# Kernel tuning notes

Hardware: AMD Instinct MI355X
Metric: run time of the kernel (lower is better)

The kernel has to match this reference:

```python
import jax, jax.numpy as jnp
import numpy as np

INPUT_SHIFT = 0.1
K = 3  # extract_image_patches(x, 3) hardcodes 3x3 patches


def extract_image_patches(x, k):
    # x: [B, C, H, W] -> [B, k*k*C, Ho, Wo], patch ordering (kh, kw, C)
    B, C, H, W = x.shape
    Ho, Wo = H - k + 1, W - k + 1
    slices = [x[:, :, i:i + Ho, j:j + Wo] for i in range(k) for j in range(k)]
    return jnp.concatenate(slices, axis=1)


def smooth_max(z, axis):
    # SMorph smooth maximum: sum(z * softmax(z)) along axis
    w = jax.nn.softmax(z, axis=axis)
    return jnp.sum(z * w, axis=axis)


def _branch(logp, kflat):
    # logp: [B, P, Ho, Wo]; kflat: [P, O] -> [B, O, Ho, Wo]
    z = logp[:, :, None] + kflat[None, :, :, None, None]  # [B, P, O, Ho, Wo]
    return jnp.exp(smooth_max(z, axis=1))


def setup_inputs() -> dict:
    key = jax.random.key(0)
    kx, kk1, kk2 = jax.random.split(key, 3)
    B, C, H, W, O = 4, 32, 32, 32, 64
    fan_in = K * K * C
    fan_out = K * K * O
    limit = float(np.sqrt(6.0 / (fan_in + fan_out)))  # xavier_uniform
    x = jax.random.normal(kx, (B, C, H, W), dtype=jnp.float32)
    k1 = jax.random.uniform(kk1, (K, K, C, O), minval=-limit, maxval=limit, dtype=jnp.float32)
    k2 = jax.random.uniform(kk2, (K, K, C, O), minval=-limit, maxval=limit, dtype=jnp.float32)
    bias = jnp.zeros((O,), dtype=jnp.float32)
    return {"x": x, "k1": k1, "k2": k2, "bias": bias}


def reference(x, k1, k2, bias):
    kh, kw, C, O = k1.shape
    k1f = k1.reshape(kh * kw * C, O)
    k2f = k2.reshape(kh * kw * C, O)
    # log of clamped patches for +x and -x
    p1 = jnp.log(jnp.maximum(extract_image_patches(x, K), INPUT_SHIFT))
    p2 = jnp.log(jnp.maximum(extract_image_patches(-x, K), INPUT_SHIFT))
    y11 = _branch(p1, k1f)
    y12 = _branch(p1, k2f)
    y21 = _branch(p2, k1f)
    y22 = _branch(p2, k2f)
    return y11 - y12 - y21 + y22 + bias[None, :, None, None]
```

## Files before the change

### kernel.cpp

```cpp
#include <hip/hip_runtime.h>
#include <math.h>


typedef float  f32x4 __attribute__((ext_vector_type(4)));
typedef short  s16x8 __attribute__((ext_vector_type(8)));

#define BB   4
#define CC   32
#define HH   32
#define WW   32
#define OO   64
#define HO   30
#define WO   30
#define NSP  900
#define KDIM 576

#define T1   131072
#define T2   (T1 + 518400)
#define T3   (T2 + 18432)

__device__ __forceinline__ unsigned short f2bf(float f) {
    unsigned u = __float_as_uint(f);
    return (unsigned short)((u + 0x7FFFu + ((u >> 16) & 1u)) >> 16);
}

__global__ __launch_bounds__(256) void smorph_prep(
    const float* __restrict__ x, const float* __restrict__ k1,
    const float* __restrict__ k2, float4* __restrict__ pixs,
    uint4* __restrict__ A3, unsigned short* __restrict__ bt)
{
    const int t = blockIdx.x * 256 + threadIdx.x;

    if (t < T1) {
        const int pix = t >> 5, c = t & 31;
        const int b = pix >> 10, h = (pix >> 5) & 31, w = pix & 31;
        float v = x[b*32768 + c*1024 + h*32 + w];
        float mp = fmaxf(v, 0.1f), mn = fmaxf(-v, 0.1f);
        float lp = mp * logf(mp), ln_ = mn * logf(mn);
        float s0 = mp, s1 = lp, s2 = mn, s3 = ln_;
#pragma unroll
        for (int m = 16; m >= 1; m >>= 1) {
            s0 += __shfl_xor(s0, m); s1 += __shfl_xor(s1, m);
            s2 += __shfl_xor(s2, m); s3 += __shfl_xor(s3, m);
        }
        if (c == 0) pixs[pix] = make_float4(s0, s1, s2, s3);
    } else if (t < T2) {
        const int u   = t - T1;
        const int mt  = u / 2304, rem = u - mt*2304;
        const int st  = rem >> 7, rem2 = rem & 127;
        const int mi  = rem2 >> 6, l = rem2 & 63;
        const int lr  = l & 15, lg = l >> 4;
        const int s   = mt*16 + mi*8 + (lr >> 1);
        const int sign = lr & 1;
        const int pos = st >> 1, khalf = st & 1;
        const int kh  = pos / 3, kw = pos - 3*(pos/3);
        const int b   = s / NSP, r = s - b*NSP;
        const int ho  = r / WO,  wo = r - WO*(r/WO);
        const int h   = ho + kh, w = wo + kw;
        const int c0  = khalf*16 + lg*4;
        const int base = b*32768 + h*32 + w;
        unsigned pk[4];
#pragma unroll
        for (int q = 0; q < 4; ++q) {
            float v = x[base + (c0 + q)*1024];
            float m = sign ? fmaxf(-v, 0.1f) : fmaxf(v, 0.1f);
            pk[q] = (unsigned)f2bf(m) | ((unsigned)f2bf(m * __logf(m)) << 16);
        }
        A3[u] = make_uint4(pk[0], pk[1], pk[2], pk[3]);
    } else if (t < T3) {
        const int u3 = t - T2;
        const int o = u3 & 63, p = u3 >> 6;
        const float a = k1[u3], b2 = k2[u3];
        const float d1 = expm1f(a),  q1 = a  * expf(a);
        const float d2 = expm1f(b2), q2 = b2 * expf(b2);
        const float vals[4][2] = {{d1, 0.f}, {q1, d1}, {d2, 0.f}, {q2, d2}};
#pragma unroll
        for (int tbl = 0; tbl < 4; ++tbl) {
            const int n = o*4 + tbl;
#pragma unroll
            for (int ks = 0; ks < 2; ++ks) {
                const int k    = 2*p + ks;
                const int st   = k >> 5, k32 = k & 31;
                const int lane = (n & 15) + ((k32 >> 3) << 4);
                bt[((n >> 4)*18 + st)*512 + lane*8 + (k32 & 7)] = f2bf(vals[tbl][ks]);
            }
        }
    }
}

__global__ __launch_bounds__(256, 2) void smorph_gemm(
    const uint4* __restrict__ A3, const unsigned short* __restrict__ bt,
    const float4* __restrict__ pixs, const float* __restrict__ bias,
    float* __restrict__ out)
{
    __shared__ float cmb[2][2048];
    __shared__ __align__(16) float epi[2][32*66];

    const int tid = threadIdx.x;
    const int l   = tid & 63;
    const int w   = tid >> 6;
    const int kq  = w >> 1;
    const int nhf = w & 1;
    const int bm  = blockIdx.x >> 1;
    const int nh  = blockIdx.x & 1;
    const int N0  = nh*128 + nhf*64;
    const int ng0 = N0 >> 4;

    const int lr = l & 15;
    const int lg = l >> 4;

    float4 S;
    {
        const int s  = bm*16 + lr;
        const int b  = s / NSP, r = s - b*NSP;
        const int ho = r / WO,  wo = r - WO*(r/WO);
        const float4* P = pixs + (b*1024 + ho*32 + wo);
        float4 a = make_float4(0,0,0,0);
#pragma unroll
        for (int kh = 0; kh < 3; ++kh)
#pragma unroll
            for (int kw = 0; kw < 3; ++kw) {
                float4 v = P[kh*32 + kw];
                a.x += v.x; a.y += v.y; a.z += v.z; a.w += v.w;
            }
        S = a;
    }

    const uint4* Ap = A3 + ((size_t)bm*18)*128 + l;
    const char*  pb = (const char*)bt;

    f32x4 acc[2][4] = {};

#pragma unroll
    for (int s2 = 0; s2 < 9; ++s2) {
        const int step = s2*2 + kq;
        s16x8 a0 = *(const s16x8*)(Ap + (step*2 + 0)*64);
        s16x8 a1 = *(const s16x8*)(Ap + (step*2 + 1)*64);
        s16x8 b0 = *(const s16x8*)(pb + (((ng0+0)*18 + step)*64 + l)*16);
        s16x8 b1 = *(const s16x8*)(pb + (((ng0+1)*18 + step)*64 + l)*16);
        s16x8 b2 = *(const s16x8*)(pb + (((ng0+2)*18 + step)*64 + l)*16);
        s16x8 b3 = *(const s16x8*)(pb + (((ng0+3)*18 + step)*64 + l)*16);

        acc[0][0] = __builtin_amdgcn_mfma_f32_16x16x32_bf16(a0, b0, acc[0][0], 0, 0, 0);
        acc[0][1] = __builtin_amdgcn_mfma_f32_16x16x32_bf16(a0, b1, acc[0][1], 0, 0, 0);
        acc[0][2] = __builtin_amdgcn_mfma_f32_16x16x32_bf16(a0, b2, acc[0][2], 0, 0, 0);
        acc[0][3] = __builtin_amdgcn_mfma_f32_16x16x32_bf16(a0, b3, acc[0][3], 0, 0, 0);
        acc[1][0] = __builtin_amdgcn_mfma_f32_16x16x32_bf16(a1, b0, acc[1][0], 0, 0, 0);
        acc[1][1] = __builtin_amdgcn_mfma_f32_16x16x32_bf16(a1, b1, acc[1][1], 0, 0, 0);
        acc[1][2] = __builtin_amdgcn_mfma_f32_16x16x32_bf16(a1, b2, acc[1][2], 0, 0, 0);
        acc[1][3] = __builtin_amdgcn_mfma_f32_16x16x32_bf16(a1, b3, acc[1][3], 0, 0, 0);
    }

    if (kq == 1) {
#pragma unroll
        for (int mi = 0; mi < 2; ++mi)
#pragma unroll
            for (int ni = 0; ni < 4; ++ni)
#pragma unroll
                for (int r = 0; r < 4; ++r)
                    cmb[nhf][(mi*16 + ni*4 + r)*64 + l] = acc[mi][ni][r];
    }
    __syncthreads();
    if (kq == 0) {
#pragma unroll
        for (int mi = 0; mi < 2; ++mi)
#pragma unroll
            for (int ni = 0; ni < 4; ++ni)
#pragma unroll
                for (int r = 0; r < 4; ++r)
                    acc[mi][ni][r] += cmb[nhf][(mi*16 + ni*4 + r)*64 + l];

        const int wrbase = lg*4*66 + lr;
#pragma unroll
        for (int mi = 0; mi < 2; ++mi)
#pragma unroll
            for (int ni = 0; ni < 4; ++ni)
#pragma unroll
                for (int r = 0; r < 4; ++r)
                    epi[nhf][wrbase + (mi*16 + r)*66 + ni*16] = acc[mi][ni][r];
    }
    __syncthreads();

    if (kq == 0) {
        const int sl = lr;
        const int oq = lg;
        const int s  = bm*16 + sl;
        const int b  = s / NSP;
        const int r900 = s - b*NSP;
#pragma unroll
        for (int oi = 0; oi < 4; ++oi) {
            int ol = oq*4 + oi;
            int o  = (N0 >> 2) + ol;
            float4 v0 = *(const float4*)&epi[nhf][(2*sl + 0)*66 + ol*4];
            float4 v1 = *(const float4*)&epi[nhf][(2*sl + 1)*66 + ol*4];
            float d1p = S.x + v0.x, n1p = S.y + v0.y;
            float d2p = S.x + v0.z, n2p = S.y + v0.w;
            float d1n = S.z + v1.x, n1n = S.w + v1.y;
            float d2n = S.z + v1.z, n2n = S.w + v1.w;
            float P = __expf(n1p/d1p) - __expf(n2p/d2p)
                    - __expf(n1n/d1n) + __expf(n2n/d2n);
            out[((size_t)(b*OO + o))*NSP + r900] = P + bias[o];
        }
    }
}

extern "C" void kernel_launch(void* const* d_in, const int* in_sizes, int n_in,
                              void* d_out, int out_size, void* d_ws, size_t ws_size,
                              hipStream_t stream) {
    const float* x    = (const float*)d_in[0];
    const float* k1   = (const float*)d_in[1];
    const float* k2   = (const float*)d_in[2];
    const float* bias = (const float*)d_in[3];

    char* ws = (char*)d_ws;
    float4*         pixs = (float4*)(ws);
    uint4*          A3   = (uint4*)(ws + 0x10000);
    unsigned short* bt   = (unsigned short*)(ws + 0x7F9000);
    float*          out  = (float*)d_out;

    hipLaunchKernelGGL(smorph_prep, dim3((T3 + 255)/256), dim3(256), 0, stream,
                       x, k1, k2, pixs, A3, bt);
    hipLaunchKernelGGL(smorph_gemm, dim3(450), dim3(256), 0, stream,
                       A3, bt, pixs, bias, out);
}
```

Measured before the change: 20.78 us.

## Build A operand in LDS inside GEMM kernel instead of global staging buffer

The A-matrix packing (clamped values and m*log m in bf16) moves out of the prep kernel. Each GEMM block now builds its tile directly from x into shared memory, so the large A3 workspace no longer round-trips through global memory. Blocks double to 512 threads, with waves split across two M sub-tiles, so each wave keeps only 4 accumulators. The cost is that each block redoes its x gathers and log computations, and the GEMM gains an extra barrier before its main loop.

```diff
diff --git a/kernel.cpp b/kernel.cpp
--- a/kernel.cpp
+++ b/kernel.cpp
@@ -16,8 +16,7 @@
 #define KDIM 576
 
 #define T1   131072
-#define T2   (T1 + 518400)
-#define T3   (T2 + 18432)
+#define TB   18432
 
 __device__ __forceinline__ unsigned short f2bf(float f) {
     unsigned u = __float_as_uint(f);
@@ -27,7 +26,7 @@
 __global__ __launch_bounds__(256) void smorph_prep(
     const float* __restrict__ x, const float* __restrict__ k1,
     const float* __restrict__ k2, float4* __restrict__ pixs,
-    uint4* __restrict__ A3, unsigned short* __restrict__ bt)
+    unsigned short* __restrict__ bt)
 {
     const int t = blockIdx.x * 256 + threadIdx.x;
 
@@ -44,31 +43,8 @@
             s2 += __shfl_xor(s2, m); s3 += __shfl_xor(s3, m);
         }
         if (c == 0) pixs[pix] = make_float4(s0, s1, s2, s3);
-    } else if (t < T2) {
-        const int u   = t - T1;
-        const int mt  = u / 2304, rem = u - mt*2304;
-        const int st  = rem >> 7, rem2 = rem & 127;
-        const int mi  = rem2 >> 6, l = rem2 & 63;
-        const int lr  = l & 15, lg = l >> 4;
-        const int s   = mt*16 + mi*8 + (lr >> 1);
-        const int sign = lr & 1;
-        const int pos = st >> 1, khalf = st & 1;
-        const int kh  = pos / 3, kw = pos - 3*(pos/3);
-        const int b   = s / NSP, r = s - b*NSP;
-        const int ho  = r / WO,  wo = r - WO*(r/WO);
-        const int h   = ho + kh, w = wo + kw;
-        const int c0  = khalf*16 + lg*4;
-        const int base = b*32768 + h*32 + w;
-        unsigned pk[4];
-#pragma unroll
-        for (int q = 0; q < 4; ++q) {
-            float v = x[base + (c0 + q)*1024];
-            float m = sign ? fmaxf(-v, 0.1f) : fmaxf(v, 0.1f);
-            pk[q] = (unsigned)f2bf(m) | ((unsigned)f2bf(m * __logf(m)) << 16);
-        }
-        A3[u] = make_uint4(pk[0], pk[1], pk[2], pk[3]);
-    } else if (t < T3) {
-        const int u3 = t - T2;
+    } else if (t < T1 + TB) {
+        const int u3 = t - T1;
         const int o = u3 & 63, p = u3 >> 6;
         const float a = k1[u3], b2 = k2[u3];
         const float d1 = expm1f(a),  q1 = a  * expf(a);
@@ -88,26 +64,49 @@
     }
 }
 
-__global__ __launch_bounds__(256, 2) void smorph_gemm(
-    const uint4* __restrict__ A3, const unsigned short* __restrict__ bt,
+__global__ __launch_bounds__(512, 4) void smorph_gemm(
+    const float* __restrict__ x, const unsigned short* __restrict__ bt,
     const float4* __restrict__ pixs, const float* __restrict__ bias,
     float* __restrict__ out)
 {
-    __shared__ float cmb[2][2048];
-    __shared__ __align__(16) float epi[2][32*66];
-
-    const int tid = threadIdx.x;
-    const int l   = tid & 63;
-    const int w   = tid >> 6;
-    const int kq  = w >> 1;
-    const int nhf = w & 1;
-    const int bm  = blockIdx.x >> 1;
-    const int nh  = blockIdx.x & 1;
-    const int N0  = nh*128 + nhf*64;
-    const int ng0 = N0 >> 4;
-
-    const int lr = l & 15;
-    const int lg = l >> 4;
+    __shared__ __align__(16) uint4 ldsA[2304];
+    float* cmb = (float*)ldsA;
+    float* epi = (float*)(ldsA + 1024);
+
+    const int tid  = threadIdx.x;
+    const int l    = tid & 63;
+    const int w    = tid >> 6;
+    const int kq   = w >> 2;
+    const int nhf  = (w >> 1) & 1;
+    const int msub = w & 1;
+    const int bm   = blockIdx.x >> 1;
+    const int nh   = blockIdx.x & 1;
+    const int N0   = nh*128 + nhf*64;
+    const int ng0  = N0 >> 4;
+    const int lr   = l & 15;
+    const int lg   = l >> 4;
+
+    for (int u = tid; u < 2304; u += 512) {
+        const int st  = u >> 7, r2 = u & 127;
+        const int mi  = r2 >> 6, l2 = r2 & 63;
+        const int lr2 = l2 & 15, lg2 = l2 >> 4;
+        const int s    = bm*16 + mi*8 + (lr2 >> 1);
+        const int sign = lr2 & 1;
+        const int pos = st >> 1, khalf = st & 1;
+        const int kh  = pos/3, kw = pos - 3*(pos/3);
+        const int b   = s / NSP, r = s - b*NSP;
+        const int ho  = r / WO,  wo = r - WO*(r/WO);
+        const int base = b*32768 + (ho + kh)*32 + (wo + kw);
+        const int c0   = khalf*16 + lg2*4;
+        unsigned pk[4];
+#pragma unroll
+        for (int q = 0; q < 4; ++q) {
+            float v = x[base + (c0 + q)*1024];
+            float m = sign ? fmaxf(-v, 0.1f) : fmaxf(v, 0.1f);
+            pk[q] = (unsigned)f2bf(m) | ((unsigned)f2bf(m * __logf(m)) << 16);
+        }
+        ldsA[u] = make_uint4(pk[0], pk[1], pk[2], pk[3]);
+    }
 
     float4 S;
     {
@@ -126,73 +125,69 @@
         S = a;
     }
 
-    const uint4* Ap = A3 + ((size_t)bm*18)*128 + l;
+    __syncthreads();
+
     const char*  pb = (const char*)bt;
-
-    f32x4 acc[2][4] = {};
+    const uint4* Al = ldsA + msub*64 + l;
+
+    f32x4 acc[4] = {};
 
 #pragma unroll
     for (int s2 = 0; s2 < 9; ++s2) {
         const int step = s2*2 + kq;
-        s16x8 a0 = *(const s16x8*)(Ap + (step*2 + 0)*64);
-        s16x8 a1 = *(const s16x8*)(Ap + (step*2 + 1)*64);
+        s16x8 a0 = *(const s16x8*)(Al + step*128);
         s16x8 b0 = *(const s16x8*)(pb + (((ng0+0)*18 + step)*64 + l)*16);
         s16x8 b1 = *(const s16x8*)(pb + (((ng0+1)*18 + step)*64 + l)*16);
         s16x8 b2 = *(const s16x8*)(pb + (((ng0+2)*18 + step)*64 + l)*16);
         s16x8 b3 = *(const s16x8*)(pb + (((ng0+3)*18 + step)*64 + l)*16);
 
-        acc[0][0] = __builtin_amdgcn_mfma_f32_16x16x32_bf16(a0, b0, acc[0][0], 0, 0, 0);
-        acc[0][1] = __builtin_amdgcn_mfma_f32_16x16x32_bf16(a0, b1, acc[0][1], 0, 0, 0);
-        acc[0][2] = __builtin_amdgcn_mfma_f32_16x16x32_bf16(a0, b2, acc[0][2], 0, 0, 0);
-        acc[0][3] = __builtin_amdgcn_mfma_f32_16x16x32_bf16(a0, b3, acc[0][3], 0, 0, 0);
-        acc[1][0] = __builtin_amdgcn_mfma_f32_16x16x32_bf16(a1, b0, acc[1][0], 0, 0, 0);
-        acc[1][1] = __builtin_amdgcn_mfma_f32_16x16x32_bf16(a1, b1, acc[1][1], 0, 0, 0);
-        acc[1][2] = __builtin_amdgcn_mfma_f32_16x16x32_bf16(a1, b2, acc[1][2], 0, 0, 0);
-        acc[1][3] = __builtin_amdgcn_mfma_f32_16x16x32_bf16(a1, b3, acc[1][3], 0, 0, 0);
-    }
+        acc[0] = __builtin_amdgcn_mfma_f32_16x16x32_bf16(a0, b0, acc[0], 0, 0, 0);
+        acc[1] = __builtin_amdgcn_mfma_f32_16x16x32_bf16(a0, b1, acc[1], 0, 0, 0);
+        acc[2] = __builtin_amdgcn_mfma_f32_16x16x32_bf16(a0, b2, acc[2], 0, 0, 0);
+        acc[3] = __builtin_amdgcn_mfma_f32_16x16x32_bf16(a0, b3, acc[3], 0, 0, 0);
+    }
+
+    __syncthreads();
 
     if (kq == 1) {
-#pragma unroll
-        for (int mi = 0; mi < 2; ++mi)
-#pragma unroll
-            for (int ni = 0; ni < 4; ++ni)
-#pragma unroll
-                for (int r = 0; r < 4; ++r)
-                    cmb[nhf][(mi*16 + ni*4 + r)*64 + l] = acc[mi][ni][r];
+        float* dst = cmb + (nhf*2 + msub)*1024 + l;
+#pragma unroll
+        for (int ni = 0; ni < 4; ++ni)
+#pragma unroll
+            for (int r = 0; r < 4; ++r)
+                dst[(ni*4 + r)*64] = acc[ni][r];
     }
     __syncthreads();
     if (kq == 0) {
-#pragma unroll
-        for (int mi = 0; mi < 2; ++mi)
-#pragma unroll
-            for (int ni = 0; ni < 4; ++ni)
-#pragma unroll
-                for (int r = 0; r < 4; ++r)
-                    acc[mi][ni][r] += cmb[nhf][(mi*16 + ni*4 + r)*64 + l];
-
-        const int wrbase = lg*4*66 + lr;
-#pragma unroll
-        for (int mi = 0; mi < 2; ++mi)
-#pragma unroll
-            for (int ni = 0; ni < 4; ++ni)
-#pragma unroll
-                for (int r = 0; r < 4; ++r)
-                    epi[nhf][wrbase + (mi*16 + r)*66 + ni*16] = acc[mi][ni][r];
-    }
-    __syncthreads();
-
-    if (kq == 0) {
+        const float* srcp = cmb + (nhf*2 + msub)*1024 + l;
+#pragma unroll
+        for (int ni = 0; ni < 4; ++ni)
+#pragma unroll
+            for (int r = 0; r < 4; ++r)
+                acc[ni][r] += srcp[(ni*4 + r)*64];
+
+        float* E = epi + nhf*2112;
+        const int wrbase = (msub*16 + lg*4)*66 + lr;
+#pragma unroll
+        for (int ni = 0; ni < 4; ++ni)
+#pragma unroll
+            for (int r = 0; r < 4; ++r)
+                E[wrbase + r*66 + ni*16] = acc[ni][r];
+    }
+    __syncthreads();
+
+    if (kq == 0 && msub == 0) {
+        const float* E = epi + nhf*2112;
         const int sl = lr;
-        const int oq = lg;
         const int s  = bm*16 + sl;
         const int b  = s / NSP;
         const int r900 = s - b*NSP;
 #pragma unroll
         for (int oi = 0; oi < 4; ++oi) {
-            int ol = oq*4 + oi;
+            int ol = lg*4 + oi;
             int o  = (N0 >> 2) + ol;
-            float4 v0 = *(const float4*)&epi[nhf][(2*sl + 0)*66 + ol*4];
-            float4 v1 = *(const float4*)&epi[nhf][(2*sl + 1)*66 + ol*4];
+            float4 v0 = *(const float4*)&E[(2*sl + 0)*66 + ol*4];
+            float4 v1 = *(const float4*)&E[(2*sl + 1)*66 + ol*4];
             float d1p = S.x + v0.x, n1p = S.y + v0.y;
             float d2p = S.x + v0.z, n2p = S.y + v0.w;
             float d1n = S.z + v1.x, n1n = S.w + v1.y;
@@ -214,12 +209,11 @@
 
     char* ws = (char*)d_ws;
     float4*         pixs = (float4*)(ws);
-    uint4*          A3   = (uint4*)(ws + 0x10000);
-    unsigned short* bt   = (unsigned short*)(ws + 0x7F9000);
+    unsigned short* bt   = (unsigned short*)(ws + 0x10000);
     float*          out  = (float*)d_out;
 
-    hipLaunchKernelGGL(smorph_prep, dim3((T3 + 255)/256), dim3(256), 0, stream,
-                       x, k1, k2, pixs, A3, bt);
-    hipLaunchKernelGGL(smorph_gemm, dim3(450), dim3(256), 0, stream,
-                       A3, bt, pixs, bias, out);
-}
+    hipLaunchKernelGGL(smorph_prep, dim3((T1 + TB + 255)/256), dim3(256), 0, stream,
+                       x, k1, k2, pixs, bt);
+    hipLaunchKernelGGL(smorph_gemm, dim3(450), dim3(512), 0, stream,
+                       x, bt, pixs, bias, out);
+}
```

Measured after the change: 20.94 us. No clear change (+0.8%).

## Replace materialized im2col A matrix with per-pixel bf16 table gathered in GEMM

Applied to the files above, without the earlier changes.

The prep kernel no longer writes a fully expanded im2col operand of about 8 MB. It instead stores, per pixel, a packed bf16 table of (m, m*log m) for both signs across all 32 channels. The GEMM computes per-lane pixel offsets and gathers 16-byte A fragments straight from this table using kh/kw/khalf immediates. This cuts prep work and global traffic by about 9x on the A operand, in exchange for less coalesced, gather-style A loads in the GEMM that depend on cache reuse of overlapping patches.

```diff
diff --git a/kernel.cpp b/kernel.cpp
--- a/kernel.cpp
+++ b/kernel.cpp
@@ -16,8 +16,7 @@
 #define KDIM 576
 
 #define T1   131072
-#define T2   (T1 + 518400)
-#define T3   (T2 + 18432)
+#define TB   18432
 
 __device__ __forceinline__ unsigned short f2bf(float f) {
     unsigned u = __float_as_uint(f);
@@ -27,7 +26,7 @@
 __global__ __launch_bounds__(256) void smorph_prep(
     const float* __restrict__ x, const float* __restrict__ k1,
     const float* __restrict__ k2, float4* __restrict__ pixs,
-    uint4* __restrict__ A3, unsigned short* __restrict__ bt)
+    unsigned* __restrict__ pixm, unsigned short* __restrict__ bt)
 {
     const int t = blockIdx.x * 256 + threadIdx.x;
 
@@ -37,6 +36,8 @@
         float v = x[b*32768 + c*1024 + h*32 + w];
         float mp = fmaxf(v, 0.1f), mn = fmaxf(-v, 0.1f);
         float lp = mp * logf(mp), ln_ = mn * logf(mn);
+        pixm[pix*64      + c] = (unsigned)f2bf(mp) | ((unsigned)f2bf(lp)  << 16);
+        pixm[pix*64 + 32 + c] = (unsigned)f2bf(mn) | ((unsigned)f2bf(ln_) << 16);
         float s0 = mp, s1 = lp, s2 = mn, s3 = ln_;
 #pragma unroll
         for (int m = 16; m >= 1; m >>= 1) {
@@ -44,31 +45,8 @@
             s2 += __shfl_xor(s2, m); s3 += __shfl_xor(s3, m);
         }
         if (c == 0) pixs[pix] = make_float4(s0, s1, s2, s3);
-    } else if (t < T2) {
-        const int u   = t - T1;
-        const int mt  = u / 2304, rem = u - mt*2304;
-        const int st  = rem >> 7, rem2 = rem & 127;
-        const int mi  = rem2 >> 6, l = rem2 & 63;
-        const int lr  = l & 15, lg = l >> 4;
-        const int s   = mt*16 + mi*8 + (lr >> 1);
-        const int sign = lr & 1;
-        const int pos = st >> 1, khalf = st & 1;
-        const int kh  = pos / 3, kw = pos - 3*(pos/3);
-        const int b   = s / NSP, r = s - b*NSP;
-        const int ho  = r / WO,  wo = r - WO*(r/WO);
-        const int h   = ho + kh, w = wo + kw;
-        const int c0  = khalf*16 + lg*4;
-        const int base = b*32768 + h*32 + w;
-        unsigned pk[4];
-#pragma unroll
-        for (int q = 0; q < 4; ++q) {
-            float v = x[base + (c0 + q)*1024];
-            float m = sign ? fmaxf(-v, 0.1f) : fmaxf(v, 0.1f);
-            pk[q] = (unsigned)f2bf(m) | ((unsigned)f2bf(m * __logf(m)) << 16);
-        }
-        A3[u] = make_uint4(pk[0], pk[1], pk[2], pk[3]);
-    } else if (t < T3) {
-        const int u3 = t - T2;
+    } else if (t < T1 + TB) {
+        const int u3 = t - T1;
         const int o = u3 & 63, p = u3 >> 6;
         const float a = k1[u3], b2 = k2[u3];
         const float d1 = expm1f(a),  q1 = a  * expf(a);
@@ -89,7 +67,7 @@
 }
 
 __global__ __launch_bounds__(256, 2) void smorph_gemm(
-    const uint4* __restrict__ A3, const unsigned short* __restrict__ bt,
+    const unsigned* __restrict__ pixm, const unsigned short* __restrict__ bt,
     const float4* __restrict__ pixs, const float* __restrict__ bias,
     float* __restrict__ out)
 {
@@ -126,16 +104,34 @@
         S = a;
     }
 
-    const uint4* Ap = A3 + ((size_t)bm*18)*128 + l;
-    const char*  pb = (const char*)bt;
+    unsigned offA[2];
+    {
+        const int sign = lr & 1;
+#pragma unroll
+        for (int mi = 0; mi < 2; ++mi) {
+            const int s  = bm*16 + mi*8 + (lr >> 1);
+            const int b  = s / NSP, r = s - b*NSP;
+            const int ho = r / WO,  wo = r - WO*(r/WO);
+            const int pix = b*1024 + ho*32 + wo;
+            offA[mi] = (unsigned)(pix*256 + sign*128 + lg*16);
+        }
+    }
+
+    const char* pa = (const char*)pixm;
+    const char* pb = (const char*)bt;
 
     f32x4 acc[2][4] = {};
 
 #pragma unroll
     for (int s2 = 0; s2 < 9; ++s2) {
-        const int step = s2*2 + kq;
-        s16x8 a0 = *(const s16x8*)(Ap + (step*2 + 0)*64);
-        s16x8 a1 = *(const s16x8*)(Ap + (step*2 + 1)*64);
+        const int step  = s2*2 + kq;
+        const int khkw  = step >> 1;
+        const int kh    = khkw / 3, kw = khkw - 3*(khkw/3);
+        const int khalf = step & 1;
+        const unsigned immA = (unsigned)(kh*8192 + kw*256 + khalf*64);
+
+        s16x8 a0 = *(const s16x8*)(pa + (offA[0] + immA));
+        s16x8 a1 = *(const s16x8*)(pa + (offA[1] + immA));
         s16x8 b0 = *(const s16x8*)(pb + (((ng0+0)*18 + step)*64 + l)*16);
         s16x8 b1 = *(const s16x8*)(pb + (((ng0+1)*18 + step)*64 + l)*16);
         s16x8 b2 = *(const s16x8*)(pb + (((ng0+2)*18 + step)*64 + l)*16);
@@ -183,13 +179,12 @@
 
     if (kq == 0) {
         const int sl = lr;
-        const int oq = lg;
         const int s  = bm*16 + sl;
         const int b  = s / NSP;
         const int r900 = s - b*NSP;
 #pragma unroll
         for (int oi = 0; oi < 4; ++oi) {
-            int ol = oq*4 + oi;
+            int ol = lg*4 + oi;
             int o  = (N0 >> 2) + ol;
             float4 v0 = *(const float4*)&epi[nhf][(2*sl + 0)*66 + ol*4];
             float4 v1 = *(const float4*)&epi[nhf][(2*sl + 1)*66 + ol*4];
@@ -214,12 +209,12 @@
 
     char* ws = (char*)d_ws;
     float4*         pixs = (float4*)(ws);
-    uint4*          A3   = (uint4*)(ws + 0x10000);
-    unsigned short* bt   = (unsigned short*)(ws + 0x7F9000);
+    unsigned*       pixm = (unsigned*)(ws + 0x10000);
+    unsigned short* bt   = (unsigned short*)(ws + 0x110000);
     float*          out  = (float*)d_out;
 
-    hipLaunchKernelGGL(smorph_prep, dim3((T3 + 255)/256), dim3(256), 0, stream,
-                       x, k1, k2, pixs, A3, bt);
+    hipLaunchKernelGGL(smorph_prep, dim3((T1 + TB + 255)/256), dim3(256), 0, stream,
+                       x, k1, k2, pixs, pixm, bt);
     hipLaunchKernelGGL(smorph_gemm, dim3(450), dim3(256), 0, stream,
-                       A3, bt, pixs, bias, out);
-}
+                       pixm, bt, pixs, bias, out);
+}
```

After: 19.75 us. 4.9% less time.
